# Optimization experiments

Measured on AMD Instinct MI355X. Metric: run time of the kernel, lower is better.

Reference implementation:

```python
import jax, jax.numpy as jnp
import numpy as np

B, C, H, W = 2, 512, 64, 64
NUM_HEADS = 8
HEAD_DIM = C // NUM_HEADS


def setup_inputs() -> dict:
    key = jax.random.key(0)
    ks = jax.random.split(key, 6)
    s = 1.0 / np.sqrt(C)
    return {
        "x": jax.random.normal(ks[0], (B, C, H, W), dtype=jnp.float32),
        "w_qkv": jax.random.normal(ks[1], (3 * C, C), dtype=jnp.float32) * s,
        "b_qkv": jax.random.normal(ks[2], (3 * C,), dtype=jnp.float32) * 0.01,
        "w_out": jax.random.normal(ks[3], (C, C), dtype=jnp.float32) * s,
        "b_out": jax.random.normal(ks[4], (C,), dtype=jnp.float32) * 0.01,
        "gamma": jax.random.normal(ks[5], (1,), dtype=jnp.float32) * 0.1,
    }


def reference(x, w_qkv, b_qkv, w_out, b_out, gamma):
    b, c, h, w = x.shape
    n = h * w
    nh, hd = NUM_HEADS, HEAD_DIM
    # 1x1 conv QKV projection == per-pixel linear
    qkv = jnp.einsum('oc,bchw->bohw', w_qkv, x) + b_qkv[None, :, None, None]
    qkv = qkv.reshape(b, 3, nh, hd, n)  # [B,3,nh,hd,N]
    q = qkv[:, 0].transpose(0, 1, 3, 2)  # [B,nh,N,hd]
    k = qkv[:, 1]                        # [B,nh,hd,N]
    v = qkv[:, 2].transpose(0, 1, 3, 2)  # [B,nh,N,hd]
    scale = hd ** -0.5
    attn = jnp.einsum('bhnd,bhdm->bhnm', q, k) * scale  # [B,nh,N,N]
    attn = jax.nn.softmax(attn, axis=-1)
    out = jnp.einsum('bhnm,bhmd->bhnd', attn, v)  # [B,nh,N,hd]
    out = out.transpose(0, 1, 3, 2).reshape(b, c, h, w)  # [B,C,H,W]
    out = jnp.einsum('oc,bchw->bohw', w_out, out) + b_out[None, :, None, None]
    return gamma[0] * out + x
```

## Files before the change

### kernel.cpp

```cpp
#include <hip/hip_runtime.h>
#include <hip/hip_bf16.h>

typedef __bf16 bf16_t;
typedef __bf16 bf16x8 __attribute__((ext_vector_type(8)));
typedef __bf16 bf16x4 __attribute__((ext_vector_type(4)));
typedef float floatx4 __attribute__((ext_vector_type(4)));
typedef float f32x16 __attribute__((ext_vector_type(16)));

#define MFMA_BF16(a, b, c) __builtin_amdgcn_mfma_f32_16x16x32_bf16((a), (b), (c), 0, 0, 0)
#define MFMA32(a, b, c) __builtin_amdgcn_mfma_f32_32x32x16_bf16((a), (b), (c), 0, 0, 0)

static constexpr int CB = 512;
static constexpr int NB = 4096;

__device__ __forceinline__ unsigned cvtpk_bf16(float lo, float hi_) {
  unsigned r;
  asm("v_cvt_pk_bf16_f32 %0, %1, %2" : "=v"(r) : "v"(lo), "v"(hi_));
  return r;
}
__device__ __forceinline__ void plswap(unsigned& x, unsigned& y) {
  asm volatile("v_permlane32_swap_b32 %0, %1" : "+v"(x), "+v"(y));
}
__device__ __forceinline__ float exp2_fast(float x) {
  float r;
  asm("v_exp_f32 %0, %1" : "=v"(r) : "v"(x));
  return r;
}
__device__ __forceinline__ void dot2_bf16(float& d, unsigned a, unsigned b) {
  asm("v_dot2_f32_bf16 %0, %1, %2, %0" : "+v"(d) : "v"(a), "v"(b));
}

#define GLOAD_LDS16(gsrc, ldst)                                              \
  __builtin_amdgcn_global_load_lds(                                          \
      (const __attribute__((address_space(1))) void*)(gsrc),                 \
      (__attribute__((address_space(3))) void*)(ldst), 16, 0, 0)

__global__ __launch_bounds__(256) void k_prep(const float* __restrict__ x,
                                              bf16_t* __restrict__ xT,
                                              const float* __restrict__ w_qkv,
                                              const float* __restrict__ w_out,
                                              bf16_t* __restrict__ Wb,
                                              bf16_t* __restrict__ Wo) {
  const int t = threadIdx.x;
  if (blockIdx.y >= 8) {
    const int widx = (blockIdx.z * 4 + (blockIdx.y - 8)) * 64 + blockIdx.x;
    const int idx = (widx * 256 + t) * 8;
    const float* src;
    bf16_t* dst;
    if (idx < 786432) { src = w_qkv + idx; dst = Wb + idx; }
    else              { src = w_out + (idx - 786432); dst = Wo + (idx - 786432); }
    const float4 a = *reinterpret_cast<const float4*>(src);
    const float4 b = *reinterpret_cast<const float4*>(src + 4);
    union { unsigned u[4]; bf16x8 v; } o;
    o.u[0] = cvtpk_bf16(a.x, a.y);
    o.u[1] = cvtpk_bf16(a.z, a.w);
    o.u[2] = cvtpk_bf16(b.x, b.y);
    o.u[3] = cvtpk_bf16(b.z, b.w);
    *reinterpret_cast<bf16x8*>(dst) = o.v;
    return;
  }
  __shared__ __align__(16) bf16_t T[64 * 72];
  const int b = blockIdx.z, c0 = blockIdx.y * 64, n0 = blockIdx.x * 64;
  {
    const int cl = t >> 4, nl = (t & 15) * 4;
#pragma unroll
    for (int p = 0; p < 4; ++p) {
      const int c = cl + p * 16;
      const float4 v = *reinterpret_cast<const float4*>(
          x + ((size_t)(b * CB + c0 + c) * NB) + n0 + nl);
      T[(nl + 0) * 72 + c] = (bf16_t)v.x;
      T[(nl + 1) * 72 + c] = (bf16_t)v.y;
      T[(nl + 2) * 72 + c] = (bf16_t)v.z;
      T[(nl + 3) * 72 + c] = (bf16_t)v.w;
    }
  }
  __syncthreads();
  {
    const int nr = t >> 2, ch = t & 3;
    bf16_t* op = xT + ((size_t)(b * NB + n0 + nr) * CB) + c0;
#pragma unroll
    for (int p = 0; p < 2; ++p) {
      bf16x8 v = *reinterpret_cast<const bf16x8*>(&T[nr * 72 + ch * 8 + p * 32]);
      *reinterpret_cast<bf16x8*>(op + ch * 8 + p * 32) = v;
    }
  }
}

__global__ __launch_bounds__(256, 2) void k_qkv(const bf16_t* __restrict__ Wb,
                                                const float* __restrict__ bias,
                                                const bf16_t* __restrict__ xT,
                                                bf16_t* __restrict__ Qb,
                                                bf16_t* __restrict__ Kb,
                                                bf16_t* __restrict__ Vb) {
  __shared__ __align__(16) bf16_t As[2][128 * 64];
  __shared__ __align__(16) bf16_t Bs[2][128 * 64];
  const int t = threadIdx.x, lane = t & 63, w = t >> 6;
  const int g = lane >> 4, c = lane & 15;
  const int wm = w >> 1, wn = w & 1;
  const int o0 = blockIdx.x * 128, n0 = blockIdx.y * 128;
  const int b = blockIdx.z;

  floatx4 acc[4][4] = {};

  const int srow = t >> 3;
  const int gch = (t & 7) ^ (srow & 7);
  const bf16_t* asrc = Wb + (size_t)(o0 + srow) * CB + gch * 8;
  const bf16_t* bsrc = xT + ((size_t)(b * NB + n0 + srow)) * CB + gch * 8;

#define QSTAGE(kt_, bufi)                                                     \
  do {                                                                        \
    _Pragma("unroll")                                                         \
    for (int p = 0; p < 4; ++p) {                                             \
      GLOAD_LDS16(asrc + (size_t)p * 32 * CB + (kt_),                         \
                  &As[(bufi)][w * 512 + p * 2048]);                           \
      GLOAD_LDS16(bsrc + (size_t)p * 32 * CB + (kt_),                         \
                  &Bs[(bufi)][w * 512 + p * 2048]);                           \
    }                                                                         \
  } while (0)

  int cho[2];
  cho[0] = (g ^ (c & 7)) * 8;
  cho[1] = ((4 + g) ^ (c & 7)) * 8;

  QSTAGE(0, 0);
  asm volatile("s_waitcnt vmcnt(0)" ::: "memory");
  __builtin_amdgcn_s_barrier();
  __builtin_amdgcn_sched_barrier(0);

  int buf = 0;
  for (int s = 0; s < 8; ++s) {
    if (s < 7) QSTAGE((s + 1) * 64, buf ^ 1);
#pragma unroll
    for (int ksub = 0; ksub < 2; ++ksub) {
      bf16x8 af[4], bfr[4];
#pragma unroll
      for (int i = 0; i < 4; ++i)
        af[i] = *reinterpret_cast<const bf16x8*>(
            &As[buf][(wm * 64 + i * 16 + c) * 64 + cho[ksub]]);
#pragma unroll
      for (int j = 0; j < 4; ++j)
        bfr[j] = *reinterpret_cast<const bf16x8*>(
            &Bs[buf][(wn * 64 + j * 16 + c) * 64 + cho[ksub]]);
#pragma unroll
      for (int i = 0; i < 4; ++i)
#pragma unroll
        for (int j = 0; j < 4; ++j)
          acc[i][j] = MFMA_BF16(af[i], bfr[j], acc[i][j]);
    }
    if (s < 7) {
      asm volatile("s_waitcnt vmcnt(0) lgkmcnt(0)" ::: "memory");
      __builtin_amdgcn_s_barrier();
      __builtin_amdgcn_sched_barrier(0);
      buf ^= 1;
    }
  }
#undef QSTAGE

  const int which = o0 >> 9;
#pragma unroll
  for (int i = 0; i < 4; ++i) {
    const int ob = o0 + wm * 64 + i * 16 + 4 * g;
    float bias4[4];
#pragma unroll
    for (int r = 0; r < 4; ++r) bias4[r] = bias[ob + r];
    const int h = (ob >> 6) & 7;
    const int d0 = ob & 63;
#pragma unroll
    for (int j = 0; j < 4; ++j) {
      const int n = n0 + wn * 64 + j * 16 + c;
      if (which == 2) {
        bf16_t* vp = Vb + (size_t)(b * 8 + h) * 64 * NB + n;
#pragma unroll
        for (int r = 0; r < 4; ++r)
          vp[(size_t)(d0 + r) * NB] = (bf16_t)(acc[i][j][r] + bias4[r]);
      } else {
        bf16_t* qp = (which == 0 ? Qb : Kb) + ((size_t)(b * 8 + h) * NB + n) * 64 + d0;
        bf16x4 pk;
#pragma unroll
        for (int r = 0; r < 4; ++r) pk[r] = (bf16_t)(acc[i][j][r] + bias4[r]);
        *reinterpret_cast<bf16x4*>(qp) = pk;
      }
    }
  }
}

__global__ __launch_bounds__(256, 2) void k_attn(const bf16_t* __restrict__ Qb,
                                                 const bf16_t* __restrict__ Kb,
                                                 const bf16_t* __restrict__ Vb,
                                                 bf16_t* __restrict__ P0,
                                                 bf16_t* __restrict__ P1,
                                                 float* __restrict__ lsum) {
  __shared__ __align__(16) bf16_t Kl[2][2][4096];
  __shared__ __align__(16) bf16_t Vl[2][2][4096];
  const int t = threadIdx.x, lane = t & 63, w = t >> 6;
  const int q31 = lane & 31, hi = lane >> 5;

  const int bid = blockIdx.x;
  const int xcd = bid & 7, j = bid >> 3;
  const int bh = xcd * 2 + (j >> 6);
  const int rest = j & 63;
  const int qt = rest >> 1, half = rest & 1;
  const int q0 = qt * 128 + w * 32;
  const int kvbase = half * 2048;

  const size_t base = (size_t)bh * NB * 64;
  const bf16_t* Qp = Qb + base;
  const bf16_t* Kp = Kb + base;
  const bf16_t* Vp = Vb + base;
  bf16_t* Op = (half ? P1 : P0) + base;

  const float SC = 0.125f * 1.44269504088896340736f;
  const float FM = 8.0f;

  bf16x8 qf[4];
#pragma unroll
  for (int ks = 0; ks < 4; ++ks) {
    bf16x8 q = *reinterpret_cast<const bf16x8*>(Qp + (size_t)(q0 + q31) * 64 + ks * 16 + hi * 8);
#pragma unroll
    for (int e = 0; e < 8; ++e) q[e] = (bf16_t)((float)q[e] * SC);
    qf[ks] = q;
  }

  const unsigned ONE2 = 0x3F803F80u;

  const int srow0 = t >> 3, srow1 = srow0 + 32;
  const int sc0 = ((t & 7) ^ (srow0 & 7)) * 8;
  const int sc1 = ((t & 7) ^ (srow1 & 7)) * 8;
  const bf16_t* ksrc0 = Kp + (size_t)(kvbase + srow0) * 64 + sc0;
  const bf16_t* ksrc1 = Kp + (size_t)(kvbase + srow1) * 64 + sc1;
  const bf16_t* vsrc0 = Vp + (size_t)srow0 * NB + kvbase + sc0;
  const bf16_t* vsrc1 = Vp + (size_t)srow1 * NB + kvbase + sc1;

#define STAGE128(ss, bufi)                                                    \
  do {                                                                        \
    const size_t ko_ = (size_t)(ss) * 8192;                                   \
    const int vo_ = (ss) * 128;                                               \
    bf16_t* kd0_ = &Kl[(bufi)][0][0];                                         \
    bf16_t* kd1_ = &Kl[(bufi)][1][0];                                         \
    bf16_t* vd0_ = &Vl[(bufi)][0][0];                                         \
    bf16_t* vd1_ = &Vl[(bufi)][1][0];                                         \
    GLOAD_LDS16(ksrc0 + ko_, kd0_ + w * 512);                                 \
    GLOAD_LDS16(ksrc1 + ko_, kd0_ + 2048 + w * 512);                          \
    GLOAD_LDS16(ksrc0 + ko_ + 4096, kd1_ + w * 512);                          \
    GLOAD_LDS16(ksrc1 + ko_ + 4096, kd1_ + 2048 + w * 512);                   \
    GLOAD_LDS16(vsrc0 + vo_, vd0_ + w * 512);                                 \
    GLOAD_LDS16(vsrc1 + vo_, vd0_ + 2048 + w * 512);                          \
    GLOAD_LDS16(vsrc0 + vo_ + 64, vd1_ + w * 512);                            \
    GLOAD_LDS16(vsrc1 + vo_ + 64, vd1_ + 2048 + w * 512);                     \
  } while (0)

  int c16r[4];
#pragma unroll
  for (int ks = 0; ks < 4; ++ks) c16r[ks] = ((ks * 2 + hi) ^ (q31 & 7)) * 8;

  f32x16 O0 = {}, O1 = {};
  float lp0 = 0.f, lp1 = 0.f, lp2 = 0.f, lp3 = 0.f;
  f32x16 NEGM;
#pragma unroll
  for (int r = 0; r < 16; ++r) NEGM[r] = -FM;

  STAGE128(0, 0);
  asm volatile("s_waitcnt vmcnt(0)" ::: "memory");
  __builtin_amdgcn_s_barrier();
  __builtin_amdgcn_sched_barrier(0);

  int buf = 0;
  for (int s = 0; s < 16; ++s) {
    if (s < 15) STAGE128(s + 1, buf ^ 1);
#pragma unroll
    for (int sub = 0; sub < 2; ++sub) {
      const bf16_t* Kbuf = &Kl[buf][sub][0];
      const bf16_t* Vbuf = &Vl[buf][sub][0];
      f32x16 st0 = NEGM, st1 = NEGM;
      __builtin_amdgcn_s_setprio(1);
#pragma unroll
      for (int ks = 0; ks < 4; ++ks) {
        bf16x8 kf0 = *reinterpret_cast<const bf16x8*>(&Kbuf[q31 * 64 + c16r[ks]]);
        bf16x8 kf1 = *reinterpret_cast<const bf16x8*>(&Kbuf[(32 + q31) * 64 + c16r[ks]]);
        st0 = MFMA32(kf0, qf[ks], st0);
        st1 = MFMA32(kf1, qf[ks], st1);
      }
      __builtin_amdgcn_s_setprio(0);

#pragma unroll
      for (int r = 0; r < 16; ++r) st0[r] = exp2_fast(st0[r]);
#pragma unroll
      for (int r = 0; r < 16; ++r) st1[r] = exp2_fast(st1[r]);

      __builtin_amdgcn_s_setprio(1);
#pragma unroll
      for (int ks = 0; ks < 4; ++ks) {
        const f32x16& P = (ks < 2) ? st0 : st1;
        const int rb = (ks & 1) * 8;
        unsigned x0 = cvtpk_bf16(P[rb + 0], P[rb + 1]);
        unsigned y0 = cvtpk_bf16(P[rb + 4], P[rb + 5]);
        unsigned x1 = cvtpk_bf16(P[rb + 2], P[rb + 3]);
        unsigned y1 = cvtpk_bf16(P[rb + 6], P[rb + 7]);
        plswap(x0, y0);
        plswap(x1, y1);
        union { unsigned u[4]; bf16x8 v; } pa;
        pa.u[0] = x0; pa.u[1] = x1; pa.u[2] = y0; pa.u[3] = y1;
        dot2_bf16(lp0, pa.u[0], ONE2);
        dot2_bf16(lp1, pa.u[1], ONE2);
        dot2_bf16(lp2, pa.u[2], ONE2);
        dot2_bf16(lp3, pa.u[3], ONE2);
        bf16x8 vf0 = *reinterpret_cast<const bf16x8*>(&Vbuf[q31 * 64 + c16r[ks]]);
        bf16x8 vf1 = *reinterpret_cast<const bf16x8*>(&Vbuf[(32 + q31) * 64 + c16r[ks]]);
        O0 = MFMA32(pa.v, vf0, O0);
        O1 = MFMA32(pa.v, vf1, O1);
      }
      __builtin_amdgcn_s_setprio(0);
    }
    if (s < 15) {
      asm volatile("s_waitcnt vmcnt(0) lgkmcnt(0)" ::: "memory");
      __builtin_amdgcn_s_barrier();
      __builtin_amdgcn_sched_barrier(0);
    }
    buf ^= 1;
  }
#undef STAGE128

#pragma unroll
  for (int r = 0; r < 16; ++r) {
    const int n = q0 + (r & 3) + 8 * (r >> 2) + 4 * hi;
    bf16_t* op = Op + ((size_t)n) * 64 + q31;
    op[0]  = (bf16_t)O0[r];
    op[32] = (bf16_t)O1[r];
  }
  {
    float lfin = (lp0 + lp1) + (lp2 + lp3);
    lfin += __shfl_xor(lfin, 32);
    if (hi == 0) {
      float* lp_ = lsum + (size_t)(half * 16 + bh) * NB;
      lp_[q0 + q31] = lfin;
    }
  }
}

__global__ __launch_bounds__(256) void k_out(const bf16_t* __restrict__ Wo,
                                             const float* __restrict__ bias,
                                             const bf16_t* __restrict__ P0,
                                             const bf16_t* __restrict__ P1,
                                             const float* __restrict__ lsum,
                                             const float* __restrict__ x,
                                             const float* __restrict__ gamma,
                                             float* __restrict__ y) {
  __shared__ __align__(16) bf16_t As[128 * 64];
  __shared__ __align__(16) bf16_t Bs[128 * 40];
  const int t = threadIdx.x;
  const int lane = t & 63, w = t >> 6;
  const int g = lane >> 4, c = lane & 15;
  const int wm = w >> 1, wn = w & 1;
  const int o0 = blockIdx.x * 128, n0 = blockIdx.y * 128;
  const int b = blockIdx.z;

  floatx4 acc[4][4] = {};

  const int srow = t >> 3;
  const int gch = (t & 7) ^ (srow & 7);
  const bf16_t* asrc = Wo + (size_t)(o0 + srow) * CB + gch * 8;

  for (int kt = 0; kt < CB; kt += 32) {
    if ((kt & 63) == 0) {
#pragma unroll
      for (int p = 0; p < 4; ++p)
        GLOAD_LDS16(asrc + (size_t)p * 32 * CB + kt, &As[w * 512 + p * 2048]);
    }
    {
      const int row = t >> 2, ch = t & 3;
      const int cc = kt + ch * 8;
      const int h = cc >> 6, d = cc & 63;
#pragma unroll
      for (int p = 0; p < 2; ++p) {
        const int r = row + p * 64;
        const int n = n0 + r;
        const size_t li = (size_t)(b * 8 + h) * NB + n;
        const size_t idx = li * 64 + d;
        const bf16x8 oa = *reinterpret_cast<const bf16x8*>(P0 + idx);
        const bf16x8 ob = *reinterpret_cast<const bf16x8*>(P1 + idx);
        const float rl = 1.0f / (lsum[li] + lsum[li + 16 * NB]);
        bf16x8 o;
#pragma unroll
        for (int e = 0; e < 8; ++e)
          o[e] = (bf16_t)(((float)oa[e] + (float)ob[e]) * rl);
        *reinterpret_cast<bf16x8*>(&Bs[r * 40 + ch * 8]) = o;
      }
    }
    __syncthreads();
    const int ksub = (kt >> 5) & 1;
    const int acho = ((ksub * 4 + g) ^ (c & 7)) * 8;
    bf16x8 af[4], bfr[4];
#pragma unroll
    for (int i = 0; i < 4; ++i)
      af[i] = *reinterpret_cast<const bf16x8*>(&As[(wm * 64 + i * 16 + c) * 64 + acho]);
#pragma unroll
    for (int j = 0; j < 4; ++j)
      bfr[j] = *reinterpret_cast<const bf16x8*>(&Bs[(wn * 64 + j * 16 + c) * 40 + g * 8]);
#pragma unroll
    for (int i = 0; i < 4; ++i)
#pragma unroll
      for (int j = 0; j < 4; ++j)
        acc[i][j] = MFMA_BF16(af[i], bfr[j], acc[i][j]);
    __syncthreads();
  }

  const float gm = gamma[0];
#pragma unroll
  for (int i = 0; i < 4; ++i) {
    const int ob = o0 + wm * 64 + i * 16 + 4 * g;
    float bias4[4];
#pragma unroll
    for (int r = 0; r < 4; ++r) bias4[r] = bias[ob + r];
#pragma unroll
    for (int j = 0; j < 4; ++j) {
      const int n = n0 + wn * 64 + j * 16 + c;
      const float* xp = x + ((size_t)(b * CB + ob) * NB) + n;
      float* yp = y + ((size_t)(b * CB + ob) * NB) + n;
#pragma unroll
      for (int r = 0; r < 4; ++r)
        yp[(size_t)r * NB] = gm * (acc[i][j][r] + bias4[r]) + xp[(size_t)r * NB];
    }
  }
}

extern "C" void kernel_launch(void* const* d_in, const int* in_sizes, int n_in,
                              void* d_out, int out_size, void* d_ws, size_t ws_size,
                              hipStream_t stream) {
  const float* x      = (const float*)d_in[0];
  const float* w_qkv  = (const float*)d_in[1];
  const float* b_qkv  = (const float*)d_in[2];
  const float* w_out  = (const float*)d_in[3];
  const float* b_out  = (const float*)d_in[4];
  const float* gamma  = (const float*)d_in[5];
  float* y = (float*)d_out;

  const size_t CH = 4194304;
  bf16_t* Wp = (bf16_t*)d_ws;
  bf16_t* Qb = Wp;
  bf16_t* Kb = Wp + CH;
  bf16_t* Vb = Wp + 2 * CH;
  bf16_t* P1 = Wp + 3 * CH;
  bf16_t* xT = Wp + 4 * CH;
  bf16_t* P0 = Wp + 4 * CH;
  bf16_t* Wb = Wp + 5 * CH;
  bf16_t* Wo = Wb + 786432;
  float*  lsum = (float*)(Wo + 262144);

  k_prep<<<dim3(64, 12, 2), 256, 0, stream>>>(x, xT, w_qkv, w_out, Wb, Wo);
  k_qkv<<<dim3(12, 32, 2), 256, 0, stream>>>(Wb, b_qkv, xT, Qb, Kb, Vb);
  k_attn<<<dim3(1024), 256, 0, stream>>>(Qb, Kb, Vb, P0, P1, lsum);
  k_out<<<dim3(4, 32, 2), 256, 0, stream>>>(Wo, b_out, P0, P1, lsum, x, gamma, y);
}
```

Baseline: 136.5 us.

## Drop LDS staging in attention; load K/V fragments directly from global memory

Removes the double-buffered LDS staging of K and V tiles and its barriers. Each wave now reads its K and V MFMA fragments straight from global memory, 32 keys per iteration, relying on L2/L1 caching for reuse across the four waves. Launch bounds are raised to 4 blocks per CU for more latency hiding. This trades shared-memory reuse and synchronisation for redundant global loads and a higher risk of memory-latency stalls.

```diff
diff --git a/kernel.cpp b/kernel.cpp
--- a/kernel.cpp
+++ b/kernel.cpp
@@ -184,14 +184,12 @@
   }
 }
 
-__global__ __launch_bounds__(256, 2) void k_attn(const bf16_t* __restrict__ Qb,
+__global__ __launch_bounds__(256, 4) void k_attn(const bf16_t* __restrict__ Qb,
                                                  const bf16_t* __restrict__ Kb,
                                                  const bf16_t* __restrict__ Vb,
                                                  bf16_t* __restrict__ P0,
                                                  bf16_t* __restrict__ P1,
                                                  float* __restrict__ lsum) {
-  __shared__ __align__(16) bf16_t Kl[2][2][4096];
-  __shared__ __align__(16) bf16_t Vl[2][2][4096];
   const int t = threadIdx.x, lane = t & 63, w = t >> 6;
   const int q31 = lane & 31, hi = lane >> 5;
 
@@ -205,8 +203,6 @@
 
   const size_t base = (size_t)bh * NB * 64;
   const bf16_t* Qp = Qb + base;
-  const bf16_t* Kp = Kb + base;
-  const bf16_t* Vp = Vb + base;
   bf16_t* Op = (half ? P1 : P0) + base;
 
   const float SC = 0.125f * 1.44269504088896340736f;
@@ -223,35 +219,9 @@
 
   const unsigned ONE2 = 0x3F803F80u;
 
-  const int srow0 = t >> 3, srow1 = srow0 + 32;
-  const int sc0 = ((t & 7) ^ (srow0 & 7)) * 8;
-  const int sc1 = ((t & 7) ^ (srow1 & 7)) * 8;
-  const bf16_t* ksrc0 = Kp + (size_t)(kvbase + srow0) * 64 + sc0;
-  const bf16_t* ksrc1 = Kp + (size_t)(kvbase + srow1) * 64 + sc1;
-  const bf16_t* vsrc0 = Vp + (size_t)srow0 * NB + kvbase + sc0;
-  const bf16_t* vsrc1 = Vp + (size_t)srow1 * NB + kvbase + sc1;
-
-#define STAGE128(ss, bufi)                                                    \
-  do {                                                                        \
-    const size_t ko_ = (size_t)(ss) * 8192;                                   \
-    const int vo_ = (ss) * 128;                                               \
-    bf16_t* kd0_ = &Kl[(bufi)][0][0];                                         \
-    bf16_t* kd1_ = &Kl[(bufi)][1][0];                                         \
-    bf16_t* vd0_ = &Vl[(bufi)][0][0];                                         \
-    bf16_t* vd1_ = &Vl[(bufi)][1][0];                                         \
-    GLOAD_LDS16(ksrc0 + ko_, kd0_ + w * 512);                                 \
-    GLOAD_LDS16(ksrc1 + ko_, kd0_ + 2048 + w * 512);                          \
-    GLOAD_LDS16(ksrc0 + ko_ + 4096, kd1_ + w * 512);                          \
-    GLOAD_LDS16(ksrc1 + ko_ + 4096, kd1_ + 2048 + w * 512);                   \
-    GLOAD_LDS16(vsrc0 + vo_, vd0_ + w * 512);                                 \
-    GLOAD_LDS16(vsrc1 + vo_, vd0_ + 2048 + w * 512);                          \
-    GLOAD_LDS16(vsrc0 + vo_ + 64, vd1_ + w * 512);                            \
-    GLOAD_LDS16(vsrc1 + vo_ + 64, vd1_ + 2048 + w * 512);                     \
-  } while (0)
-
-  int c16r[4];
-#pragma unroll
-  for (int ks = 0; ks < 4; ++ks) c16r[ks] = ((ks * 2 + hi) ^ (q31 & 7)) * 8;
+  const bf16_t* kp  = Kb + base + (size_t)(kvbase + q31) * 64 + hi * 8;
+  const bf16_t* vp0 = Vb + base + (size_t)q31 * NB + kvbase + hi * 8;
+  const bf16_t* vp1 = vp0 + (size_t)32 * NB;
 
   f32x16 O0 = {}, O1 = {};
   float lp0 = 0.f, lp1 = 0.f, lp2 = 0.f, lp3 = 0.f;
@@ -259,66 +229,66 @@
 #pragma unroll
   for (int r = 0; r < 16; ++r) NEGM[r] = -FM;
 
-  STAGE128(0, 0);
-  asm volatile("s_waitcnt vmcnt(0)" ::: "memory");
-  __builtin_amdgcn_s_barrier();
-  __builtin_amdgcn_sched_barrier(0);
-
-  int buf = 0;
-  for (int s = 0; s < 16; ++s) {
-    if (s < 15) STAGE128(s + 1, buf ^ 1);
-#pragma unroll
-    for (int sub = 0; sub < 2; ++sub) {
-      const bf16_t* Kbuf = &Kl[buf][sub][0];
-      const bf16_t* Vbuf = &Vl[buf][sub][0];
-      f32x16 st0 = NEGM, st1 = NEGM;
-      __builtin_amdgcn_s_setprio(1);
-#pragma unroll
-      for (int ks = 0; ks < 4; ++ks) {
-        bf16x8 kf0 = *reinterpret_cast<const bf16x8*>(&Kbuf[q31 * 64 + c16r[ks]]);
-        bf16x8 kf1 = *reinterpret_cast<const bf16x8*>(&Kbuf[(32 + q31) * 64 + c16r[ks]]);
-        st0 = MFMA32(kf0, qf[ks], st0);
-        st1 = MFMA32(kf1, qf[ks], st1);
-      }
-      __builtin_amdgcn_s_setprio(0);
-
-#pragma unroll
-      for (int r = 0; r < 16; ++r) st0[r] = exp2_fast(st0[r]);
-#pragma unroll
-      for (int r = 0; r < 16; ++r) st1[r] = exp2_fast(st1[r]);
-
-      __builtin_amdgcn_s_setprio(1);
-#pragma unroll
-      for (int ks = 0; ks < 4; ++ks) {
-        const f32x16& P = (ks < 2) ? st0 : st1;
-        const int rb = (ks & 1) * 8;
-        unsigned x0 = cvtpk_bf16(P[rb + 0], P[rb + 1]);
-        unsigned y0 = cvtpk_bf16(P[rb + 4], P[rb + 5]);
-        unsigned x1 = cvtpk_bf16(P[rb + 2], P[rb + 3]);
-        unsigned y1 = cvtpk_bf16(P[rb + 6], P[rb + 7]);
-        plswap(x0, y0);
-        plswap(x1, y1);
-        union { unsigned u[4]; bf16x8 v; } pa;
-        pa.u[0] = x0; pa.u[1] = x1; pa.u[2] = y0; pa.u[3] = y1;
-        dot2_bf16(lp0, pa.u[0], ONE2);
-        dot2_bf16(lp1, pa.u[1], ONE2);
-        dot2_bf16(lp2, pa.u[2], ONE2);
-        dot2_bf16(lp3, pa.u[3], ONE2);
-        bf16x8 vf0 = *reinterpret_cast<const bf16x8*>(&Vbuf[q31 * 64 + c16r[ks]]);
-        bf16x8 vf1 = *reinterpret_cast<const bf16x8*>(&Vbuf[(32 + q31) * 64 + c16r[ks]]);
-        O0 = MFMA32(pa.v, vf0, O0);
-        O1 = MFMA32(pa.v, vf1, O1);
-      }
-      __builtin_amdgcn_s_setprio(0);
-    }
-    if (s < 15) {
-      asm volatile("s_waitcnt vmcnt(0) lgkmcnt(0)" ::: "memory");
-      __builtin_amdgcn_s_barrier();
-      __builtin_amdgcn_sched_barrier(0);
-    }
-    buf ^= 1;
-  }
-#undef STAGE128
+#pragma unroll 2
+  for (int u = 0; u < 64; ++u) {
+    const bf16_t* ku = kp + (size_t)u * 32 * 64;
+    const bf16x8 kf0 = *reinterpret_cast<const bf16x8*>(ku);
+    const bf16x8 kf1 = *reinterpret_cast<const bf16x8*>(ku + 16);
+    const bf16x8 kf2 = *reinterpret_cast<const bf16x8*>(ku + 32);
+    const bf16x8 kf3 = *reinterpret_cast<const bf16x8*>(ku + 48);
+    f32x16 st = NEGM;
+    __builtin_amdgcn_s_setprio(1);
+    st = MFMA32(kf0, qf[0], st);
+    st = MFMA32(kf1, qf[1], st);
+    st = MFMA32(kf2, qf[2], st);
+    st = MFMA32(kf3, qf[3], st);
+    __builtin_amdgcn_s_setprio(0);
+
+    const bf16_t* vu0 = vp0 + u * 32;
+    const bf16_t* vu1 = vp1 + u * 32;
+    const bf16x8 vfa = *reinterpret_cast<const bf16x8*>(vu0);
+    const bf16x8 vfb = *reinterpret_cast<const bf16x8*>(vu0 + 16);
+    const bf16x8 vfc = *reinterpret_cast<const bf16x8*>(vu1);
+    const bf16x8 vfd = *reinterpret_cast<const bf16x8*>(vu1 + 16);
+
+#pragma unroll
+    for (int r = 0; r < 16; ++r) st[r] = exp2_fast(st[r]);
+
+    __builtin_amdgcn_s_setprio(1);
+    {
+      unsigned x0 = cvtpk_bf16(st[0], st[1]);
+      unsigned y0 = cvtpk_bf16(st[4], st[5]);
+      unsigned x1 = cvtpk_bf16(st[2], st[3]);
+      unsigned y1 = cvtpk_bf16(st[6], st[7]);
+      plswap(x0, y0);
+      plswap(x1, y1);
+      union { unsigned u4[4]; bf16x8 v; } pa;
+      pa.u4[0] = x0; pa.u4[1] = x1; pa.u4[2] = y0; pa.u4[3] = y1;
+      dot2_bf16(lp0, pa.u4[0], ONE2);
+      dot2_bf16(lp1, pa.u4[1], ONE2);
+      dot2_bf16(lp2, pa.u4[2], ONE2);
+      dot2_bf16(lp3, pa.u4[3], ONE2);
+      O0 = MFMA32(pa.v, vfa, O0);
+      O1 = MFMA32(pa.v, vfc, O1);
+    }
+    {
+      unsigned x0 = cvtpk_bf16(st[8], st[9]);
+      unsigned y0 = cvtpk_bf16(st[12], st[13]);
+      unsigned x1 = cvtpk_bf16(st[10], st[11]);
+      unsigned y1 = cvtpk_bf16(st[14], st[15]);
+      plswap(x0, y0);
+      plswap(x1, y1);
+      union { unsigned u4[4]; bf16x8 v; } pa;
+      pa.u4[0] = x0; pa.u4[1] = x1; pa.u4[2] = y0; pa.u4[3] = y1;
+      dot2_bf16(lp0, pa.u4[0], ONE2);
+      dot2_bf16(lp1, pa.u4[1], ONE2);
+      dot2_bf16(lp2, pa.u4[2], ONE2);
+      dot2_bf16(lp3, pa.u4[3], ONE2);
+      O0 = MFMA32(pa.v, vfb, O0);
+      O1 = MFMA32(pa.v, vfd, O1);
+    }
+    __builtin_amdgcn_s_setprio(0);
+  }
 
 #pragma unroll
   for (int r = 0; r < 16; ++r) {
```

After: 290.2 us. 113% more time.
